# Optimization experiments

Measured on AMD Instinct MI355X. Metric: run time of the kernel, lower is better.

## Reference

```python
import jax, jax.numpy as jnp
import numpy as np

# Swin block config (matches init_kwargs)
NUM_HEADS = 6
WS = 7          # window_size
SHIFT = 3       # shift_size
C = 192         # channels; keras MHA key_dim = channels
KEY_DIM = C


def setup_inputs() -> dict:
    key = jax.random.key(0)
    ks = jax.random.split(key, 9)
    B, H, W = 16, 112, 112
    s = 0.02
    x = jax.random.normal(ks[0], (B, H, W, C), dtype=jnp.float32)
    # keras MultiHeadAttention params: Wq/Wk/Wv [C, heads, key_dim], Wo [heads, key_dim, C]
    Wq = jax.random.normal(ks[1], (C, NUM_HEADS, KEY_DIM), dtype=jnp.float32) * s
    bq = jnp.zeros((NUM_HEADS, KEY_DIM), dtype=jnp.float32)
    Wk = jax.random.normal(ks[2], (C, NUM_HEADS, KEY_DIM), dtype=jnp.float32) * s
    bk = jnp.zeros((NUM_HEADS, KEY_DIM), dtype=jnp.float32)
    Wv = jax.random.normal(ks[3], (C, NUM_HEADS, KEY_DIM), dtype=jnp.float32) * s
    bv = jnp.zeros((NUM_HEADS, KEY_DIM), dtype=jnp.float32)
    Wo = jax.random.normal(ks[4], (NUM_HEADS, KEY_DIM, C), dtype=jnp.float32) * s
    bo = jnp.zeros((C,), dtype=jnp.float32)
    return {"x": x, "Wq": Wq, "bq": bq, "Wk": Wk, "bk": bk,
            "Wv": Wv, "bv": bv, "Wo": Wo, "bo": bo}


def reference(x, Wq, bq, Wk, bk, Wv, bv, Wo, bo):
    B, H, W, _ = x.shape
    # shifted window: roll up-left
    x = jnp.roll(x, shift=(-SHIFT, -SHIFT), axis=(1, 2))
    # window partition (== tf.image.extract_patches + reshape):
    # [B,H,W,C] -> [B*nW, ws*ws, C] with row-major window-token order
    nH, nW = H // WS, W // WS
    win = x.reshape(B, nH, WS, nW, WS, C).transpose(0, 1, 3, 2, 4, 5)
    win = win.reshape(B * nH * nW, WS * WS, C)
    q = jnp.einsum('btc,chd->bthd', win, Wq) + bq
    k = jnp.einsum('btc,chd->bthd', win, Wk) + bk
    v = jnp.einsum('btc,chd->bthd', win, Wv) + bv
    scale = 1.0 / jnp.sqrt(jnp.asarray(KEY_DIM, dtype=q.dtype))
    scores = jnp.einsum('bthd,bshd->bhts', q, k) * scale  # [nWin, heads, 49, 49]
    attn = jax.nn.softmax(scores, axis=-1)
    o = jnp.einsum('bhts,bshd->bthd', attn, v)
    o = jnp.einsum('bthd,hdc->btc', o, Wo) + bo
    # NOTE: original code merges windows with a PLAIN reshape (does not invert
    # the partition); replicate exactly for faithfulness.
    out = o.reshape(B, H, W, C)
    out = jnp.roll(out, shift=(SHIFT, SHIFT), axis=(1, 2))
    return out
```

## Files before the change

kernel.cpp:

```cpp
#include <hip/hip_runtime.h>
#include <hip/hip_bf16.h>

typedef __bf16 bf16_t;
typedef __bf16 bf16x4 __attribute__((ext_vector_type(4)));
typedef __bf16 bf16x8 __attribute__((ext_vector_type(8)));
typedef float  f32x4  __attribute__((ext_vector_type(4)));

#define NH    6
#define CH    192
#define HW    112
#define SHIFT 3

#define XLD 200
#define PLD 68

#define X_OFF   0
#define T0_OFF  9800
#define T1_OFF  19600
#define P0_OFF  29400
#define P1_OFF  33752
#define LDS_ELEMS 38104
#define LDS_BYTES (LDS_ELEMS * 2)

#define U_OFF_ELEMS  (NH * CH * CH)
#define BU_OFF_BYTES (2 * NH * CH * CH * 2)
#define W1_OFF_BYTES (BU_OFF_BYTES + NH * CH * 4)

__global__ void prep_gt(const float* __restrict__ Wq, const float* __restrict__ Wk,
                        bf16_t* __restrict__ gt) {
  __shared__ float wk_row[CH];
  int h = blockIdx.x / CH, cp = blockIdx.x % CH;
  int c = threadIdx.x;
  wk_row[c] = Wk[(cp * NH + h) * CH + c];
  __syncthreads();
  float acc = 0.f;
  for (int d = 0; d < CH; ++d)
    acc += wk_row[d] * Wq[(c * NH + h) * CH + d];
  int tile = cp >> 4, l15 = cp & 15;
  int ks = c >> 5, lg = (c >> 3) & 3, e = c & 7;
  gt[((((h * 12 + tile) * 6 + ks) << 6) + lg * 16 + l15) * 8 + e] = (bf16_t)acc;
}

__global__ void prep_u(const float* __restrict__ Wv, const float* __restrict__ Wo,
                       bf16_t* __restrict__ u_out) {
  __shared__ float wv_row[CH];
  int h = blockIdx.x / CH, ci = blockIdx.x % CH;
  int t = threadIdx.x;
  wv_row[t] = Wv[(ci * NH + h) * CH + t];
  __syncthreads();
  float acc = 0.f;
  for (int d = 0; d < CH; ++d)
    acc += wv_row[d] * Wo[(h * CH + d) * CH + t];
  int tile = t >> 4, l15 = t & 15;
  int ks = ci >> 5, lg = (ci >> 3) & 3, e = ci & 7;
  u_out[((((h * 12 + tile) * 6 + ks) << 6) + lg * 16 + l15) * 8 + e] = (bf16_t)acc;
}

__global__ void prep_bu(const float* __restrict__ bv, const float* __restrict__ Wo,
                        float* __restrict__ bu) {
  int h = blockIdx.x, c = threadIdx.x;
  float acc = 0.f;
  for (int d = 0; d < CH; ++d)
    acc += bv[h * CH + d] * Wo[(h * CH + d) * CH + c];
  bu[h * CH + c] = acc;
}

__global__ void prep_w1(const float* __restrict__ Wk, const float* __restrict__ bq,
                        float* __restrict__ w1) {
  int h = blockIdx.x, cp = threadIdx.x;
  float acc = 0.f;
  for (int d = 0; d < CH; ++d)
    acc += Wk[(cp * NH + h) * CH + d] * bq[h * CH + d];
  w1[h * CH + cp] = acc;
}

__device__ __forceinline__ void t_phase(const bf16_t* __restrict__ gt,
                                        const float* __restrict__ w1h,
                                        const bf16_t* Xl, bf16_t* Tdst,
                                        int hh, int wm, int lane, int l15, int lg) {
  f32x4 ww[3];
#pragma unroll
  for (int mi = 0; mi < 3; ++mi)
    ww[mi] = *(const f32x4*)&w1h[(wm + mi) * 16 + lg * 4];
#pragma unroll
  for (int ip = 0; ip < 2; ++ip) {
    f32x4 acc[3][2];
#pragma unroll
    for (int mi = 0; mi < 3; ++mi)
#pragma unroll
      for (int n2 = 0; n2 < 2; ++n2) acc[mi][n2] = ww[mi];
#pragma unroll
    for (int ks = 0; ks < 6; ++ks) {
      bf16x8 af[3], bfr[2];
#pragma unroll
      for (int mi = 0; mi < 3; ++mi)
        af[mi] = *(const bf16x8*)&gt[((((hh * 12 + wm + mi) * 6 + ks) << 6) + lane) * 8];
#pragma unroll
      for (int n2 = 0; n2 < 2; ++n2)
        bfr[n2] = *(const bf16x8*)&Xl[((ip * 2 + n2) * 16 + l15) * XLD + ks * 32 + lg * 8];
#pragma unroll
      for (int mi = 0; mi < 3; ++mi)
#pragma unroll
        for (int n2 = 0; n2 < 2; ++n2)
          acc[mi][n2] = __builtin_amdgcn_mfma_f32_16x16x32_bf16(af[mi], bfr[n2], acc[mi][n2], 0, 0, 0);
    }
#pragma unroll
    for (int mi = 0; mi < 3; ++mi) {
      int cp0 = (wm + mi) * 16 + lg * 4;
#pragma unroll
      for (int n2 = 0; n2 < 2; ++n2) {
        int i = (ip * 2 + n2) * 16 + l15;
        if (i < 49) {
          bf16x4 pk = { (bf16_t)acc[mi][n2][0], (bf16_t)acc[mi][n2][1],
                        (bf16_t)acc[mi][n2][2], (bf16_t)acc[mi][n2][3] };
          *(bf16x4*)&Tdst[i * XLD + cp0] = pk;
        }
      }
    }
  }
}

__global__ __launch_bounds__(256, 2) void swin_fused(
    const float* __restrict__ x,
    const float* __restrict__ bo,
    const bf16_t* __restrict__ wts,
    const float* __restrict__ bu, const float* __restrict__ w1,
    float* __restrict__ out) {
  extern __shared__ char smem_raw[];
  bf16_t* lds = (bf16_t*)smem_raw;
  bf16_t* Xl  = lds + X_OFF;

  const int tid  = threadIdx.x;
  const int wave = tid >> 6;
  const int lane = tid & 63;
  const int l15  = lane & 15;
  const int lg   = lane >> 4;

  const int blk = blockIdx.x;
  const int b   = blk >> 8;
  const int rem = blk & 255;
  const int wi  = rem >> 4, wj = rem & 15;

  for (int idx = tid; idx < 49 * 48; idx += 256) {
    int t = idx / 48, q4 = idx % 48;
    int hs = wi * 7 + t / 7 + SHIFT; if (hs >= HW) hs -= HW;
    int ws2 = wj * 7 + t % 7 + SHIFT; if (ws2 >= HW) ws2 -= HW;
    const float4 v = *(const float4*)&x[(((b * HW + hs) * HW) + ws2) * CH + q4 * 4];
    bf16x4 pk = { (bf16_t)v.x, (bf16_t)v.y, (bf16_t)v.z, (bf16_t)v.w };
    *(bf16x4*)&Xl[t * XLD + q4 * 4] = pk;
  }
  __syncthreads();

  const int wm = wave * 3;
  const float scale = 0.07216878364870322f;

  t_phase(wts, w1, Xl, lds + T0_OFF, 0, wm, lane, l15, lg);
  __syncthreads();

  f32x4 yacc[3][4] = {};

  for (int h = 0; h < NH; ++h) {
    const bf16_t* Tcur = lds + ((h & 1) ? T1_OFF : T0_OFF);
    bf16_t*       Pcur = lds + ((h & 1) ? P1_OFF : P0_OFF);

    bf16x4 psave[4];
    {
      f32x4 sacc[4] = {};
#pragma unroll
      for (int ks = 0; ks < 6; ++ks) {
        bf16x8 bt = *(const bf16x8*)&Tcur[(wave * 16 + l15) * XLD + ks * 32 + lg * 8];
#pragma unroll
        for (int mj = 0; mj < 4; ++mj) {
          bf16x8 af = *(const bf16x8*)&Xl[(mj * 16 + l15) * XLD + ks * 32 + lg * 8];
          sacc[mj] = __builtin_amdgcn_mfma_f32_16x16x32_bf16(af, bt, sacc[mj], 0, 0, 0);
        }
      }
      float p[4][4];
      float sum = 0.f;
#pragma unroll
      for (int mj = 0; mj < 3; ++mj)
#pragma unroll
        for (int r = 0; r < 4; ++r) {
          float e = __expf(sacc[mj][r] * scale);
          p[mj][r] = e;
          sum += e;
        }
      {
        float e0 = (lg == 0) ? __expf(sacc[3][0] * scale) : 0.f;
        p[3][0] = e0; p[3][1] = 0.f; p[3][2] = 0.f; p[3][3] = 0.f;
        sum += e0;
      }
      sum += __shfl_xor(sum, 16);
      sum += __shfl_xor(sum, 32);
      float inv = 1.f / sum;
#pragma unroll
      for (int mj = 0; mj < 4; ++mj) {
        bf16x4 pk = { (bf16_t)(p[mj][0] * inv), (bf16_t)(p[mj][1] * inv),
                      (bf16_t)(p[mj][2] * inv), (bf16_t)(p[mj][3] * inv) };
        psave[mj] = pk;
      }
    }
    {
      int irow = wave * 16 + l15;
#pragma unroll
      for (int mj = 0; mj < 4; ++mj)
        *(bf16x4*)&Pcur[irow * PLD + mj * 16 + lg * 4] = psave[mj];
    }
    if (h + 1 < NH)
      t_phase(wts, w1 + (h + 1) * CH, Xl, lds + (((h + 1) & 1) ? T1_OFF : T0_OFF),
              h + 1, wm, lane, l15, lg);
    bf16x8 bfrag[3][2];
    {
      const bf16_t* U_w = wts + U_OFF_ELEMS;
      const float* bu_h = bu + h * CH;
#pragma unroll
      for (int mi = 0; mi < 3; ++mi) {
        const f32x4 bbv = *(const f32x4*)&bu_h[(wm + mi) * 16 + lg * 4];
        f32x4 vacc[4];
#pragma unroll
        for (int ms = 0; ms < 4; ++ms) vacc[ms] = bbv;
#pragma unroll
        for (int ks = 0; ks < 6; ++ks) {
          bf16x8 bfu = *(const bf16x8*)&U_w[((((h * 12 + wm + mi) * 6 + ks) << 6) + lane) * 8];
#pragma unroll
          for (int ms = 0; ms < 4; ++ms) {
            bf16x8 af = *(const bf16x8*)&Xl[(ms * 16 + l15) * XLD + ks * 32 + lg * 8];
            vacc[ms] = __builtin_amdgcn_mfma_f32_16x16x32_bf16(af, bfu, vacc[ms], 0, 0, 0);
          }
        }
        if (lg) { vacc[3] = (f32x4){0.f, 0.f, 0.f, 0.f}; }
        else    { vacc[3][1] = 0.f; vacc[3][2] = 0.f; vacc[3][3] = 0.f; }
#pragma unroll
        for (int kp = 0; kp < 2; ++kp) {
          bf16x4 lo = { (bf16_t)vacc[2 * kp][0], (bf16_t)vacc[2 * kp][1],
                        (bf16_t)vacc[2 * kp][2], (bf16_t)vacc[2 * kp][3] };
          bf16x4 hi = { (bf16_t)vacc[2 * kp + 1][0], (bf16_t)vacc[2 * kp + 1][1],
                        (bf16_t)vacc[2 * kp + 1][2], (bf16_t)vacc[2 * kp + 1][3] };
          bfrag[mi][kp] = __builtin_shufflevector(lo, hi, 0, 1, 2, 3, 4, 5, 6, 7);
        }
      }
    }
    __syncthreads();
    {
#pragma unroll
      for (int ni = 0; ni < 4; ++ni) {
#pragma unroll
        for (int kp = 0; kp < 2; ++kp) {
          const bf16_t* pr = &Pcur[(ni * 16 + l15) * PLD + kp * 32 + lg * 4];
          bf16x4 a0 = *(const bf16x4*)pr;
          bf16x4 a1 = *(const bf16x4*)(pr + 16);
          bf16x8 af8 = __builtin_shufflevector(a0, a1, 0, 1, 2, 3, 4, 5, 6, 7);
#pragma unroll
          for (int mi = 0; mi < 3; ++mi)
            yacc[mi][ni] = __builtin_amdgcn_mfma_f32_16x16x32_bf16(af8, bfrag[mi][kp], yacc[mi][ni], 0, 0, 0);
        }
      }
    }
  }

  {
    float bov[3];
#pragma unroll
    for (int mi = 0; mi < 3; ++mi) bov[mi] = bo[(wm + mi) * 16 + l15];
#pragma unroll
    for (int ni = 0; ni < 4; ++ni) {
#pragma unroll
      for (int r = 0; r < 4; ++r) {
        int t = ni * 16 + lg * 4 + r;
        if (t < 49) {
          int pos = rem * 49 + t;
          int hp = pos / 112, wp = pos % 112;
          hp += SHIFT; if (hp >= HW) hp -= HW;
          wp += SHIFT; if (wp >= HW) wp -= HW;
          float* op = out + (((b * HW + hp) * HW) + wp) * CH + l15;
#pragma unroll
          for (int mi = 0; mi < 3; ++mi)
            op[(wm + mi) * 16] = yacc[mi][ni][r] + bov[mi];
        }
      }
    }
  }
}

extern "C" void kernel_launch(void* const* d_in, const int* in_sizes, int n_in,
                              void* d_out, int out_size, void* d_ws, size_t ws_size,
                              hipStream_t stream) {
  const float* x  = (const float*)d_in[0];
  const float* Wq = (const float*)d_in[1];
  const float* bq = (const float*)d_in[2];
  const float* Wk = (const float*)d_in[3];
  const float* Wv = (const float*)d_in[5];
  const float* bv = (const float*)d_in[6];
  const float* Wo = (const float*)d_in[7];
  const float* bo = (const float*)d_in[8];
  float* out = (float*)d_out;
  bf16_t* wts = (bf16_t*)d_ws;
  float*  bu  = (float*)((char*)d_ws + BU_OFF_BYTES);
  float*  w1  = (float*)((char*)d_ws + W1_OFF_BYTES);

  prep_gt<<<NH * CH, CH, 0, stream>>>(Wq, Wk, wts);
  prep_u<<<NH * CH, CH, 0, stream>>>(Wv, Wo, wts + U_OFF_ELEMS);
  prep_bu<<<NH, CH, 0, stream>>>(bv, Wo, bu);
  prep_w1<<<NH, CH, 0, stream>>>(Wk, bq, w1);

  (void)hipFuncSetAttribute((const void*)swin_fused,
                            hipFuncAttributeMaxDynamicSharedMemorySize, LDS_BYTES);
  swin_fused<<<dim3(4096), dim3(256), LDS_BYTES, stream>>>(x, bo, wts, bu, w1, out);
}
```

Measured before the change: 402.3 us.

## Split per-window work across six waves instead of four

Raises the block from 256 to 384 threads, so each of six waves owns two 16-column output/projection tiles instead of three. Only the first four waves compute the 49-row score/softmax tiles; the other two skip that phase. Launch bounds move to 384 threads with 3 blocks per CU, which aims at more resident waves and less per-wave register pressure. The cost is idle waves during the softmax phase, and LDS per block (~76KB) may cap occupancy below the 3 blocks requested.

```diff
diff --git a/kernel.cpp b/kernel.cpp
--- a/kernel.cpp
+++ b/kernel.cpp
@@ -77,36 +77,36 @@
 __device__ __forceinline__ void t_phase(const bf16_t* __restrict__ gt,
                                         const float* __restrict__ w1h,
                                         const bf16_t* Xl, bf16_t* Tdst,
-                                        int hh, int wm, int lane, int l15, int lg) {
-  f32x4 ww[3];
-#pragma unroll
-  for (int mi = 0; mi < 3; ++mi)
-    ww[mi] = *(const f32x4*)&w1h[(wm + mi) * 16 + lg * 4];
+                                        int hh, int wm2, int lane, int l15, int lg) {
+  f32x4 ww[2];
+#pragma unroll
+  for (int mi = 0; mi < 2; ++mi)
+    ww[mi] = *(const f32x4*)&w1h[(wm2 + mi) * 16 + lg * 4];
 #pragma unroll
   for (int ip = 0; ip < 2; ++ip) {
-    f32x4 acc[3][2];
-#pragma unroll
-    for (int mi = 0; mi < 3; ++mi)
+    f32x4 acc[2][2];
+#pragma unroll
+    for (int mi = 0; mi < 2; ++mi)
 #pragma unroll
       for (int n2 = 0; n2 < 2; ++n2) acc[mi][n2] = ww[mi];
 #pragma unroll
     for (int ks = 0; ks < 6; ++ks) {
-      bf16x8 af[3], bfr[2];
-#pragma unroll
-      for (int mi = 0; mi < 3; ++mi)
-        af[mi] = *(const bf16x8*)&gt[((((hh * 12 + wm + mi) * 6 + ks) << 6) + lane) * 8];
+      bf16x8 af[2], bfr[2];
+#pragma unroll
+      for (int mi = 0; mi < 2; ++mi)
+        af[mi] = *(const bf16x8*)&gt[((((hh * 12 + wm2 + mi) * 6 + ks) << 6) + lane) * 8];
 #pragma unroll
       for (int n2 = 0; n2 < 2; ++n2)
         bfr[n2] = *(const bf16x8*)&Xl[((ip * 2 + n2) * 16 + l15) * XLD + ks * 32 + lg * 8];
 #pragma unroll
-      for (int mi = 0; mi < 3; ++mi)
+      for (int mi = 0; mi < 2; ++mi)
 #pragma unroll
         for (int n2 = 0; n2 < 2; ++n2)
           acc[mi][n2] = __builtin_amdgcn_mfma_f32_16x16x32_bf16(af[mi], bfr[n2], acc[mi][n2], 0, 0, 0);
     }
 #pragma unroll
-    for (int mi = 0; mi < 3; ++mi) {
-      int cp0 = (wm + mi) * 16 + lg * 4;
+    for (int mi = 0; mi < 2; ++mi) {
+      int cp0 = (wm2 + mi) * 16 + lg * 4;
 #pragma unroll
       for (int n2 = 0; n2 < 2; ++n2) {
         int i = (ip * 2 + n2) * 16 + l15;
@@ -120,7 +120,7 @@
   }
 }
 
-__global__ __launch_bounds__(256, 2) void swin_fused(
+__global__ __launch_bounds__(384, 3) void swin_fused(
     const float* __restrict__ x,
     const float* __restrict__ bo,
     const bf16_t* __restrict__ wts,
@@ -131,7 +131,7 @@
   bf16_t* Xl  = lds + X_OFF;
 
   const int tid  = threadIdx.x;
-  const int wave = tid >> 6;
+  const int wave = tid / 64;
   const int lane = tid & 63;
   const int l15  = lane & 15;
   const int lg   = lane >> 4;
@@ -141,7 +141,7 @@
   const int rem = blk & 255;
   const int wi  = rem >> 4, wj = rem & 15;
 
-  for (int idx = tid; idx < 49 * 48; idx += 256) {
+  for (int idx = tid; idx < 49 * 48; idx += 384) {
     int t = idx / 48, q4 = idx % 48;
     int hs = wi * 7 + t / 7 + SHIFT; if (hs >= HW) hs -= HW;
     int ws2 = wj * 7 + t % 7 + SHIFT; if (ws2 >= HW) ws2 -= HW;
@@ -151,20 +151,19 @@
   }
   __syncthreads();
 
-  const int wm = wave * 3;
+  const int wm2 = wave * 2;
   const float scale = 0.07216878364870322f;
 
-  t_phase(wts, w1, Xl, lds + T0_OFF, 0, wm, lane, l15, lg);
+  t_phase(wts, w1, Xl, lds + T0_OFF, 0, wm2, lane, l15, lg);
   __syncthreads();
 
-  f32x4 yacc[3][4] = {};
+  f32x4 yacc[2][4] = {};
 
   for (int h = 0; h < NH; ++h) {
     const bf16_t* Tcur = lds + ((h & 1) ? T1_OFF : T0_OFF);
     bf16_t*       Pcur = lds + ((h & 1) ? P1_OFF : P0_OFF);
 
-    bf16x4 psave[4];
-    {
+    if (wave < 4) {
       f32x4 sacc[4] = {};
 #pragma unroll
       for (int ks = 0; ks < 6; ++ks) {
@@ -175,53 +174,47 @@
           sacc[mj] = __builtin_amdgcn_mfma_f32_16x16x32_bf16(af, bt, sacc[mj], 0, 0, 0);
         }
       }
-      float p[4][4];
       float sum = 0.f;
 #pragma unroll
       for (int mj = 0; mj < 3; ++mj)
 #pragma unroll
         for (int r = 0; r < 4; ++r) {
           float e = __expf(sacc[mj][r] * scale);
-          p[mj][r] = e;
+          sacc[mj][r] = e;
           sum += e;
         }
       {
         float e0 = (lg == 0) ? __expf(sacc[3][0] * scale) : 0.f;
-        p[3][0] = e0; p[3][1] = 0.f; p[3][2] = 0.f; p[3][3] = 0.f;
+        sacc[3][0] = e0; sacc[3][1] = 0.f; sacc[3][2] = 0.f; sacc[3][3] = 0.f;
         sum += e0;
       }
       sum += __shfl_xor(sum, 16);
       sum += __shfl_xor(sum, 32);
       float inv = 1.f / sum;
+      int irow = wave * 16 + l15;
 #pragma unroll
       for (int mj = 0; mj < 4; ++mj) {
-        bf16x4 pk = { (bf16_t)(p[mj][0] * inv), (bf16_t)(p[mj][1] * inv),
-                      (bf16_t)(p[mj][2] * inv), (bf16_t)(p[mj][3] * inv) };
-        psave[mj] = pk;
-      }
-    }
-    {
-      int irow = wave * 16 + l15;
-#pragma unroll
-      for (int mj = 0; mj < 4; ++mj)
-        *(bf16x4*)&Pcur[irow * PLD + mj * 16 + lg * 4] = psave[mj];
+        bf16x4 pk = { (bf16_t)(sacc[mj][0] * inv), (bf16_t)(sacc[mj][1] * inv),
+                      (bf16_t)(sacc[mj][2] * inv), (bf16_t)(sacc[mj][3] * inv) };
+        *(bf16x4*)&Pcur[irow * PLD + mj * 16 + lg * 4] = pk;
+      }
     }
     if (h + 1 < NH)
       t_phase(wts, w1 + (h + 1) * CH, Xl, lds + (((h + 1) & 1) ? T1_OFF : T0_OFF),
-              h + 1, wm, lane, l15, lg);
-    bf16x8 bfrag[3][2];
+              h + 1, wm2, lane, l15, lg);
+    bf16x8 bfrag[2][2];
     {
       const bf16_t* U_w = wts + U_OFF_ELEMS;
       const float* bu_h = bu + h * CH;
 #pragma unroll
-      for (int mi = 0; mi < 3; ++mi) {
-        const f32x4 bbv = *(const f32x4*)&bu_h[(wm + mi) * 16 + lg * 4];
+      for (int mi = 0; mi < 2; ++mi) {
+        const f32x4 bbv = *(const f32x4*)&bu_h[(wm2 + mi) * 16 + lg * 4];
         f32x4 vacc[4];
 #pragma unroll
         for (int ms = 0; ms < 4; ++ms) vacc[ms] = bbv;
 #pragma unroll
         for (int ks = 0; ks < 6; ++ks) {
-          bf16x8 bfu = *(const bf16x8*)&U_w[((((h * 12 + wm + mi) * 6 + ks) << 6) + lane) * 8];
+          bf16x8 bfu = *(const bf16x8*)&U_w[((((h * 12 + wm2 + mi) * 6 + ks) << 6) + lane) * 8];
 #pragma unroll
           for (int ms = 0; ms < 4; ++ms) {
             bf16x8 af = *(const bf16x8*)&Xl[(ms * 16 + l15) * XLD + ks * 32 + lg * 8];
@@ -251,7 +244,7 @@
           bf16x4 a1 = *(const bf16x4*)(pr + 16);
           bf16x8 af8 = __builtin_shufflevector(a0, a1, 0, 1, 2, 3, 4, 5, 6, 7);
 #pragma unroll
-          for (int mi = 0; mi < 3; ++mi)
+          for (int mi = 0; mi < 2; ++mi)
             yacc[mi][ni] = __builtin_amdgcn_mfma_f32_16x16x32_bf16(af8, bfrag[mi][kp], yacc[mi][ni], 0, 0, 0);
         }
       }
@@ -259,9 +252,9 @@
   }
 
   {
-    float bov[3];
-#pragma unroll
-    for (int mi = 0; mi < 3; ++mi) bov[mi] = bo[(wm + mi) * 16 + l15];
+    float bov[2];
+#pragma unroll
+    for (int mi = 0; mi < 2; ++mi) bov[mi] = bo[(wm2 + mi) * 16 + l15];
 #pragma unroll
     for (int ni = 0; ni < 4; ++ni) {
 #pragma unroll
@@ -274,8 +267,8 @@
           wp += SHIFT; if (wp >= HW) wp -= HW;
           float* op = out + (((b * HW + hp) * HW) + wp) * CH + l15;
 #pragma unroll
-          for (int mi = 0; mi < 3; ++mi)
-            op[(wm + mi) * 16] = yacc[mi][ni][r] + bov[mi];
+          for (int mi = 0; mi < 2; ++mi)
+            op[(wm2 + mi) * 16] = yacc[mi][ni][r] + bov[mi];
         }
       }
     }
@@ -305,5 +298,5 @@
 
   (void)hipFuncSetAttribute((const void*)swin_fused,
                             hipFuncAttributeMaxDynamicSharedMemorySize, LDS_BYTES);
-  swin_fused<<<dim3(4096), dim3(256), LDS_BYTES, stream>>>(x, bo, wts, bu, w1, out);
-}
+  swin_fused<<<dim3(4096), dim3(384), LDS_BYTES, stream>>>(x, bo, wts, bu, w1, out);
+}
```

Measured after the change: 878.0 us. 2.18x slower.
